# Kernel optimization log

Measured on AMD Instinct MI355X. Metric: run time of the kernel, lower is better.

Reference implementation:

```python
import jax, jax.numpy as jnp
import numpy as np

B, C_IN, C_KEY, C_VAL, C_OUT = 1, 64, 32, 64, 64
H = W = D = 64
SCALE = 8


def setup_inputs() -> dict:
    key = jax.random.key(0)
    ks = jax.random.split(key, 4)
    init = lambda k, shape, fan: jax.random.normal(k, shape, jnp.float32) * (fan ** -0.5)
    return {
        "x": jax.random.normal(ks[0], (B, C_IN, H, W, D), jnp.float32),
        "w_key": init(ks[1], (C_KEY, C_IN), C_IN),
        "b_key": jnp.zeros((C_KEY,), jnp.float32),
        "w_value": init(ks[2], (C_VAL, C_IN), C_IN),
        "b_value": jnp.zeros((C_VAL,), jnp.float32),
        "w_out": init(ks[3], (C_OUT, C_VAL), C_VAL),
        "b_out": jnp.zeros((C_OUT,), jnp.float32),
        "scale": SCALE,
    }


def _proj(t, wgt, bias):
    # 1x1x1 Conv3d == pointwise channel matmul
    return jnp.einsum('bchwd,oc->bohwd', t, wgt) + bias[None, :, None, None, None]


def _windows(t, s):
    # [B,C,H,W,D] -> [B, s^3 windows, hb*wb*db tokens, C]
    b, c, h, w, d = t.shape
    hb, wb, db = h // s, w // s, d // s
    t = t.reshape(b, c, s, hb, s, wb, s, db)
    t = t.transpose(0, 2, 4, 6, 3, 5, 7, 1)
    return t.reshape(b, s * s * s, hb * wb * db, c), (hb, wb, db)


def _unwindows(t, s, blk):
    hb, wb, db = blk
    b, c = t.shape[0], t.shape[-1]
    t = t.reshape(b, s, s, s, hb, wb, db, c)
    t = t.transpose(0, 7, 1, 4, 2, 5, 3, 6)
    return t.reshape(b, c, s * hb, s * wb, s * db)


def reference(x, w_key, b_key, w_value, b_value, w_out, b_out, scale):
    # f_query = f_key (shared module in the original)
    k_full = _proj(x, w_key, b_key)
    v_full = _proj(x, w_value, b_value)
    qw, blk = _windows(k_full, scale)
    kw = qw  # shared projection -> query == key
    vw, _ = _windows(v_full, scale)
    sim = jnp.einsum('bnlc,bnmc->bnlm', qw, kw) * (qw.shape[-1] ** -0.5)
    sim = jax.nn.softmax(sim, axis=-1)
    ctx = jnp.einsum('bnlm,bnmc->bnlc', sim, vw)
    ctx = _unwindows(ctx, scale, blk)
    return _proj(ctx, w_out, b_out)
```

## Files before the change

kernel.cpp:

```cpp
#include <hip/hip_runtime.h>

typedef unsigned short u16;
typedef __bf16 bf16x8 __attribute__((ext_vector_type(8)));
typedef float f32x16 __attribute__((ext_vector_type(16)));

union B8 { bf16x8 v; u16 s[8]; unsigned u[4]; uint4 u4; };

__device__ __forceinline__ unsigned cvtpk(float a, float b) {
    unsigned r;
    asm("v_cvt_pk_bf16_f32 %0, %1, %2" : "=v"(r) : "v"(a), "v"(b));
    return r;
}
__device__ __forceinline__ float ex2(float x) { return __builtin_amdgcn_exp2f(x); }
__device__ __forceinline__ void swap32(unsigned &a, unsigned &b) {
    asm("v_permlane32_swap_b32 %0, %1" : "+v"(a), "+v"(b));
}
__device__ __forceinline__ B8 load_w8(const float* __restrict__ p, float s) {
    float4 lo = ((const float4*)p)[0];
    float4 hi = ((const float4*)p)[1];
    B8 r;
    r.u[0] = cvtpk(lo.x * s, lo.y * s);
    r.u[1] = cvtpk(lo.z * s, lo.w * s);
    r.u[2] = cvtpk(hi.x * s, hi.y * s);
    r.u[3] = cvtpk(hi.z * s, hi.w * s);
    return r;
}
__device__ __forceinline__ f32x16 mfma32(const B8 a, const B8 b, f32x16 c) {
    return __builtin_amdgcn_mfma_f32_32x32x16_bf16(a.v, b.v, c, 0, 0, 0);
}
__device__ __forceinline__ int kidx(int row, int sl) {
    return row * 32 + (((sl ^ (row >> 1)) & 3) << 3);
}
__device__ __forceinline__ void build_b(const float* p, B8& b0, B8& b1) {
    unsigned c0 = cvtpk(p[0], p[1]),   c1 = cvtpk(p[2], p[3]);
    unsigned c2 = cvtpk(p[4], p[5]),   c3 = cvtpk(p[6], p[7]);
    unsigned c4 = cvtpk(p[8], p[9]),   c5 = cvtpk(p[10], p[11]);
    unsigned c6 = cvtpk(p[12], p[13]), c7 = cvtpk(p[14], p[15]);
    swap32(c0, c2); swap32(c1, c3); swap32(c4, c6); swap32(c5, c7);
    b0.u[0] = c0; b0.u[1] = c1; b0.u[2] = c2; b0.u[3] = c3;
    b1.u[0] = c4; b1.u[1] = c5; b1.u[2] = c6; b1.u[3] = c7;
}

#define VOFF 16384
#define XOFF 49664
#define NSM  68096

__global__ __launch_bounds__(1024, 4)
void psab_fused(const float* __restrict__ x,
                const float* __restrict__ wk, const float* __restrict__ bk,
                const float* __restrict__ wv, const float* __restrict__ bv,
                const float* __restrict__ wo, const float* __restrict__ bo,
                float* __restrict__ out)
{
    __shared__ __align__(16) u16 smem[NSM];
    const int t    = threadIdx.x;
    const int lane = t & 63;
    const int wid  = t >> 6;
    const int cl   = lane & 31;
    const int h5   = lane >> 5;

    const int bid = blockIdx.x;
    const int n   = (bid & 7) * 64 + (bid >> 3);
    const int sh = n >> 6, sw = (n >> 3) & 7, sd = n & 7;
    const size_t base_vox = (size_t)(sh * 8) * 4096 + (size_t)(sw * 8) * 64 + (size_t)(sd * 8);

    const float WSC = 0.50506330f;

    const int pair = wid >> 1;
    const int kv   = wid & 1;

    B8 wB[8];
    float bkv[16];
    float vb0 = 0.f, vb1 = 0.f;
    if (kv == 0) {
#pragma unroll
        for (int kc = 0; kc < 4; ++kc)
            wB[kc] = load_w8(wk + cl * 64 + kc * 16 + h5 * 8, WSC);
#pragma unroll
        for (int r = 0; r < 16; ++r)
            bkv[r] = bk[(r & 3) + 8 * (r >> 2) + 4 * h5] * WSC;
    } else {
#pragma unroll
        for (int nb = 0; nb < 2; ++nb)
#pragma unroll
            for (int kc = 0; kc < 4; ++kc)
                wB[nb * 4 + kc] = load_w8(wv + (nb * 32 + cl) * 64 + kc * 16 + h5 * 8, 1.0f);
        vb0 = bv[cl]; vb1 = bv[32 + cl];
    }

    const f32x16 z16 = {0,0,0,0,0,0,0,0,0,0,0,0,0,0,0,0};

    const int cS = t & 63;
    const int r3 = t >> 6;
    float4 L4[2], H4[2];
#define LDX(cc)                                                                               \
    _Pragma("unroll")                                                                         \
    for (int i = 0; i < 2; ++i) {                                                             \
        const int rr = r3 + i * 16;                                                           \
        const float* gp = x + (size_t)cS * 262144 + base_vox                                  \
                        + ((cc) * 4 + (rr >> 3)) * 4096 + (rr & 7) * 64;                      \
        L4[i] = ((const float4*)gp)[0];                                                       \
        H4[i] = ((const float4*)gp)[1];                                                       \
    }
#define STX()                                                                                 \
    _Pragma("unroll")                                                                         \
    for (int i = 0; i < 2; ++i) {                                                             \
        const int rr = r3 + i * 16;                                                           \
        unsigned a0 = cvtpk(L4[i].x, L4[i].y), a1 = cvtpk(L4[i].z, L4[i].w);                  \
        unsigned a2 = cvtpk(H4[i].x, H4[i].y), a3 = cvtpk(H4[i].z, H4[i].w);                  \
        u16* xp = &smem[XOFF + (rr * 8) * 72 + cS];                                           \
        xp[0 * 72] = (u16)a0; xp[1 * 72] = (u16)(a0 >> 16);                                   \
        xp[2 * 72] = (u16)a1; xp[3 * 72] = (u16)(a1 >> 16);                                   \
        xp[4 * 72] = (u16)a2; xp[5 * 72] = (u16)(a2 >> 16);                                   \
        xp[6 * 72] = (u16)a3; xp[7 * 72] = (u16)(a3 >> 16);                                   \
    }

    LDX(0)
    STX()
    __syncthreads();
    LDX(1)

#pragma unroll
    for (int cc = 0; cc < 2; ++cc) {
        const int tokb = cc * 256 + pair * 32;
        B8 ax[4];
#pragma unroll
        for (int kc = 0; kc < 4; ++kc)
            ax[kc].u4 = *(const uint4*)&smem[XOFF + (pair * 32 + cl) * 72 + kc * 16 + h5 * 8];
        if (kv == 0) {
            f32x16 kd = mfma32(wB[0], ax[0], z16);
            kd = mfma32(wB[1], ax[1], kd);
            kd = mfma32(wB[2], ax[2], kd);
            kd = mfma32(wB[3], ax[3], kd);
            const int trow = tokb + cl;
#pragma unroll
            for (int g = 0; g < 4; ++g) {
                uint2 pk;
                pk.x = cvtpk(kd[4 * g + 0] + bkv[4 * g + 0], kd[4 * g + 1] + bkv[4 * g + 1]);
                pk.y = cvtpk(kd[4 * g + 2] + bkv[4 * g + 2], kd[4 * g + 3] + bkv[4 * g + 3]);
                *(uint2*)&smem[kidx(trow, g) + 4 * h5] = pk;
            }
        } else {
#pragma unroll
            for (int nb = 0; nb < 2; ++nb) {
                f32x16 vd = mfma32(ax[0], wB[nb * 4 + 0], z16);
                vd = mfma32(ax[1], wB[nb * 4 + 1], vd);
                vd = mfma32(ax[2], wB[nb * 4 + 2], vd);
                vd = mfma32(ax[3], wB[nb * 4 + 3], vd);
                const int cv = nb * 32 + cl;
                const float vb = nb ? vb1 : vb0;
#pragma unroll
                for (int rq = 0; rq < 4; ++rq) {
                    uint2 pk;
                    pk.x = cvtpk(vd[rq * 4 + 0] + vb, vd[rq * 4 + 1] + vb);
                    pk.y = cvtpk(vd[rq * 4 + 2] + vb, vd[rq * 4 + 3] + vb);
                    *(uint2*)&smem[VOFF + cv * 520 + tokb + rq * 8 + 4 * h5] = pk;
                }
            }
        }
        if (cc == 0) {
            __syncthreads();
            STX()
            __syncthreads();
        }
    }
    __syncthreads();

    B8 qB[2];
#pragma unroll
    for (int kc = 0; kc < 2; ++kc)
        qB[kc].u4 = *(const uint4*)&smem[kidx(wid * 32 + cl, 2 * kc + h5)];

    f32x16 ctx0 = z16, ctx1 = z16;
    float lsum = 0.f;

#pragma unroll 2
    for (int ci = 0; ci < 16; ++ci) {
        const int m0 = ci * 32;
        B8 kA0, kA1, va00, va01, va10, va11;
        kA0.u4  = *(const uint4*)&smem[kidx(m0 + cl, h5)];
        kA1.u4  = *(const uint4*)&smem[kidx(m0 + cl, 2 + h5)];
        va00.u4 = *(const uint4*)&smem[VOFF + cl * 520 + m0 + h5 * 8];
        va01.u4 = *(const uint4*)&smem[VOFF + cl * 520 + m0 + 16 + h5 * 8];
        va10.u4 = *(const uint4*)&smem[VOFF + (32 + cl) * 520 + m0 + h5 * 8];
        va11.u4 = *(const uint4*)&smem[VOFF + (32 + cl) * 520 + m0 + 16 + h5 * 8];

        __builtin_amdgcn_s_setprio(1);
        f32x16 s = mfma32(kA0, qB[0], z16);
        s = mfma32(kA1, qB[1], s);
        __builtin_amdgcn_s_setprio(0);

        float p[16];
#pragma unroll
        for (int i = 0; i < 16; ++i) p[i] = ex2(s[i]);
        lsum += (((p[0]+p[1])+(p[2]+p[3]))+((p[4]+p[5])+(p[6]+p[7])))
              + (((p[8]+p[9])+(p[10]+p[11]))+((p[12]+p[13])+(p[14]+p[15])));
        B8 pb0, pb1;
        build_b(p, pb0, pb1);

        __builtin_amdgcn_s_setprio(1);
        ctx0 = mfma32(va00, pb0, ctx0);
        ctx0 = mfma32(va01, pb1, ctx0);
        ctx1 = mfma32(va10, pb0, ctx1);
        ctx1 = mfma32(va11, pb1, ctx1);
        __builtin_amdgcn_s_setprio(0);
    }

    lsum += __shfl_xor(lsum, 32);
    const float inv = 1.0f / lsum;

    B8 aw[2][4];
#pragma unroll
    for (int cob = 0; cob < 2; ++cob)
#pragma unroll
        for (int kc = 0; kc < 4; ++kc)
            aw[cob][kc] = load_w8(wo + (cob * 32 + cl) * 64 + kc * 16 + h5 * 8, 1.0f);

    float pn[16];
    B8 cq[4];
#pragma unroll
    for (int i = 0; i < 16; ++i) pn[i] = ctx0[i] * inv;
    build_b(pn, cq[0], cq[1]);
#pragma unroll
    for (int i = 0; i < 16; ++i) pn[i] = ctx1[i] * inv;
    build_b(pn, cq[2], cq[3]);

    __syncthreads();

    float* fout = (float*)((char*)smem + wid * 8192);
#pragma unroll
    for (int cob = 0; cob < 2; ++cob) {
        f32x16 od = mfma32(aw[cob][0], cq[0], z16);
        od = mfma32(aw[cob][1], cq[1], od);
        od = mfma32(aw[cob][2], cq[2], od);
        od = mfma32(aw[cob][3], cq[3], od);
#pragma unroll
        for (int r = 0; r < 16; ++r) {
            const int row = cob * 32 + (r & 3) + 8 * (r >> 2) + 4 * h5;
            fout[row * 32 + cl] = od[r];
        }
    }

    float* outw = out + base_vox + (size_t)(wid >> 1) * 4096 + (wid & 1) * 256;
#pragma unroll
    for (int it = 0; it < 8; ++it) {
        const int co = it * 8 + (lane >> 3);
        const int q4 = (lane & 7) * 4;
        float4 v4 = *(const float4*)&fout[co * 32 + q4];
        const float bco = bo[co];
        v4.x += bco; v4.y += bco; v4.z += bco; v4.w += bco;
        const int wb = (lane & 7) >> 1, db0 = (lane & 1) * 4;
        *(float4*)&outw[(size_t)co * 262144 + wb * 64 + db0] = v4;
    }
}

extern "C" void kernel_launch(void* const* d_in, const int* in_sizes, int n_in,
                              void* d_out, int out_size, void* d_ws, size_t ws_size,
                              hipStream_t stream) {
    const float* x  = (const float*)d_in[0];
    const float* wk = (const float*)d_in[1];
    const float* bk = (const float*)d_in[2];
    const float* wv = (const float*)d_in[3];
    const float* bv = (const float*)d_in[4];
    const float* wo = (const float*)d_in[5];
    const float* bo = (const float*)d_in[6];
    float* o = (float*)d_out;
    psab_fused<<<dim3(512), dim3(1024), 0, stream>>>(x, wk, bk, wv, bv, wo, bo, o);
}
```

Measured before the change: 74.32 us.

## Shrink blocks to four waves, each handling four query tiles with shared K/V loads

Cuts each block from 16 to 4 waves. Each wave now computes both the K and V projections for 64 tokens, and in attention it processes four 32-query tiles. This lets each K/V LDS fragment load feed four score and context MFMA groups, reducing LDS traffic per MFMA and the number of barrier participants. The X staging buffer switches from a padded stride-72 layout to an XOR-swizzled stride-64 layout, and the output writeback is restructured to match. In exchange it raises register pressure heavily (eight context accumulators, more weights held in registers) and lowers the number of waves per CU available to hide latency, with launch bounds set to 256 threads.

New measurement: 76.10 us. 1.02x slower.

```diff
diff --git a/kernel.cpp b/kernel.cpp
--- a/kernel.cpp
+++ b/kernel.cpp
@@ -43,9 +43,9 @@
 
 #define VOFF 16384
 #define XOFF 49664
-#define NSM  68096
-
-__global__ __launch_bounds__(1024, 4)
+#define NSM  66048
+
+__global__ __launch_bounds__(256, 1)
 void psab_fused(const float* __restrict__ x,
                 const float* __restrict__ wk, const float* __restrict__ bk,
                 const float* __restrict__ wv, const float* __restrict__ bv,
@@ -66,37 +66,29 @@
 
     const float WSC = 0.50506330f;
 
-    const int pair = wid >> 1;
-    const int kv   = wid & 1;
-
-    B8 wB[8];
+    B8 wkB[4], wvB[2][4];
+#pragma unroll
+    for (int kc = 0; kc < 4; ++kc)
+        wkB[kc] = load_w8(wk + cl * 64 + kc * 16 + h5 * 8, WSC);
+#pragma unroll
+    for (int nb = 0; nb < 2; ++nb)
+#pragma unroll
+        for (int kc = 0; kc < 4; ++kc)
+            wvB[nb][kc] = load_w8(wv + (nb * 32 + cl) * 64 + kc * 16 + h5 * 8, 1.0f);
     float bkv[16];
-    float vb0 = 0.f, vb1 = 0.f;
-    if (kv == 0) {
-#pragma unroll
-        for (int kc = 0; kc < 4; ++kc)
-            wB[kc] = load_w8(wk + cl * 64 + kc * 16 + h5 * 8, WSC);
-#pragma unroll
-        for (int r = 0; r < 16; ++r)
-            bkv[r] = bk[(r & 3) + 8 * (r >> 2) + 4 * h5] * WSC;
-    } else {
-#pragma unroll
-        for (int nb = 0; nb < 2; ++nb)
-#pragma unroll
-            for (int kc = 0; kc < 4; ++kc)
-                wB[nb * 4 + kc] = load_w8(wv + (nb * 32 + cl) * 64 + kc * 16 + h5 * 8, 1.0f);
-        vb0 = bv[cl]; vb1 = bv[32 + cl];
-    }
+#pragma unroll
+    for (int r = 0; r < 16; ++r)
+        bkv[r] = bk[(r & 3) + 8 * (r >> 2) + 4 * h5] * WSC;
+    const float vb0 = bv[cl], vb1 = bv[32 + cl];
 
     const f32x16 z16 = {0,0,0,0,0,0,0,0,0,0,0,0,0,0,0,0};
 
     const int cS = t & 63;
-    const int r3 = t >> 6;
-    float4 L4[2], H4[2];
+    float4 L4[8], H4[8];
 #define LDX(cc)                                                                               \
     _Pragma("unroll")                                                                         \
-    for (int i = 0; i < 2; ++i) {                                                             \
-        const int rr = r3 + i * 16;                                                           \
+    for (int i = 0; i < 8; ++i) {                                                             \
+        const int rr = wid + i * 4;                                                           \
         const float* gp = x + (size_t)cS * 262144 + base_vox                                  \
                         + ((cc) * 4 + (rr >> 3)) * 4096 + (rr & 7) * 64;                      \
         L4[i] = ((const float4*)gp)[0];                                                       \
@@ -104,15 +96,15 @@
     }
 #define STX()                                                                                 \
     _Pragma("unroll")                                                                         \
-    for (int i = 0; i < 2; ++i) {                                                             \
-        const int rr = r3 + i * 16;                                                           \
+    for (int i = 0; i < 8; ++i) {                                                             \
+        const int rr = wid + i * 4;                                                           \
         unsigned a0 = cvtpk(L4[i].x, L4[i].y), a1 = cvtpk(L4[i].z, L4[i].w);                  \
         unsigned a2 = cvtpk(H4[i].x, H4[i].y), a3 = cvtpk(H4[i].z, H4[i].w);                  \
-        u16* xp = &smem[XOFF + (rr * 8) * 72 + cS];                                           \
-        xp[0 * 72] = (u16)a0; xp[1 * 72] = (u16)(a0 >> 16);                                   \
-        xp[2 * 72] = (u16)a1; xp[3 * 72] = (u16)(a1 >> 16);                                   \
-        xp[4 * 72] = (u16)a2; xp[5 * 72] = (u16)(a2 >> 16);                                   \
-        xp[6 * 72] = (u16)a3; xp[7 * 72] = (u16)(a3 >> 16);                                   \
+        const u16 vals[8] = { (u16)a0, (u16)(a0 >> 16), (u16)a1, (u16)(a1 >> 16),             \
+                              (u16)a2, (u16)(a2 >> 16), (u16)a3, (u16)(a3 >> 16) };           \
+        _Pragma("unroll")                                                                     \
+        for (int j = 0; j < 8; ++j)                                                           \
+            smem[XOFF + (rr * 8 + j) * 64 + (((cS >> 3) ^ j) << 3) + (cS & 7)] = vals[j];     \
     }
 
     LDX(0)
@@ -122,16 +114,20 @@
 
 #pragma unroll
     for (int cc = 0; cc < 2; ++cc) {
-        const int tokb = cc * 256 + pair * 32;
-        B8 ax[4];
-#pragma unroll
-        for (int kc = 0; kc < 4; ++kc)
-            ax[kc].u4 = *(const uint4*)&smem[XOFF + (pair * 32 + cl) * 72 + kc * 16 + h5 * 8];
-        if (kv == 0) {
-            f32x16 kd = mfma32(wB[0], ax[0], z16);
-            kd = mfma32(wB[1], ax[1], kd);
-            kd = mfma32(wB[2], ax[2], kd);
-            kd = mfma32(wB[3], ax[3], kd);
+#pragma unroll
+        for (int sb = 0; sb < 2; ++sb) {
+            const int ltok = wid * 64 + sb * 32 + cl;
+            const int tokb = cc * 256 + wid * 64 + sb * 32;
+            B8 ax[4];
+#pragma unroll
+            for (int kc = 0; kc < 4; ++kc) {
+                const int slot = (kc * 2 + h5) ^ (ltok & 7);
+                ax[kc].u4 = *(const uint4*)&smem[XOFF + ltok * 64 + (slot << 3)];
+            }
+            f32x16 kd = mfma32(wkB[0], ax[0], z16);
+            kd = mfma32(wkB[1], ax[1], kd);
+            kd = mfma32(wkB[2], ax[2], kd);
+            kd = mfma32(wkB[3], ax[3], kd);
             const int trow = tokb + cl;
 #pragma unroll
             for (int g = 0; g < 4; ++g) {
@@ -140,13 +136,12 @@
                 pk.y = cvtpk(kd[4 * g + 2] + bkv[4 * g + 2], kd[4 * g + 3] + bkv[4 * g + 3]);
                 *(uint2*)&smem[kidx(trow, g) + 4 * h5] = pk;
             }
-        } else {
 #pragma unroll
             for (int nb = 0; nb < 2; ++nb) {
-                f32x16 vd = mfma32(ax[0], wB[nb * 4 + 0], z16);
-                vd = mfma32(ax[1], wB[nb * 4 + 1], vd);
-                vd = mfma32(ax[2], wB[nb * 4 + 2], vd);
-                vd = mfma32(ax[3], wB[nb * 4 + 3], vd);
+                f32x16 vd = mfma32(ax[0], wvB[nb][0], z16);
+                vd = mfma32(ax[1], wvB[nb][1], vd);
+                vd = mfma32(ax[2], wvB[nb][2], vd);
+                vd = mfma32(ax[3], wvB[nb][3], vd);
                 const int cv = nb * 32 + cl;
                 const float vb = nb ? vb1 : vb0;
 #pragma unroll
@@ -166,13 +161,31 @@
     }
     __syncthreads();
 
-    B8 qB[2];
-#pragma unroll
-    for (int kc = 0; kc < 2; ++kc)
-        qB[kc].u4 = *(const uint4*)&smem[kidx(wid * 32 + cl, 2 * kc + h5)];
-
-    f32x16 ctx0 = z16, ctx1 = z16;
-    float lsum = 0.f;
+    B8 qB[4][2];
+#pragma unroll
+    for (int qb = 0; qb < 4; ++qb)
+#pragma unroll
+        for (int kc = 0; kc < 2; ++kc)
+            qB[qb][kc].u4 = *(const uint4*)&smem[kidx(wid * 128 + qb * 32 + cl, 2 * kc + h5)];
+
+    f32x16 ctx00 = z16, ctx01 = z16, ctx10 = z16, ctx11 = z16;
+    f32x16 ctx20 = z16, ctx21 = z16, ctx30 = z16, ctx31 = z16;
+    float ls0 = 0.f, ls1 = 0.f, ls2 = 0.f, ls3 = 0.f;
+
+#define SM(qb, sv, c0, c1)                                                                    \
+    {                                                                                         \
+        float p[16];                                                                          \
+        _Pragma("unroll")                                                                     \
+        for (int i = 0; i < 16; ++i) p[i] = ex2(sv[i]);                                       \
+        ls##qb += (((p[0]+p[1])+(p[2]+p[3]))+((p[4]+p[5])+(p[6]+p[7])))                       \
+                + (((p[8]+p[9])+(p[10]+p[11]))+((p[12]+p[13])+(p[14]+p[15])));                \
+        B8 pb0, pb1;                                                                          \
+        build_b(p, pb0, pb1);                                                                 \
+        c0 = mfma32(va00, pb0, c0);                                                           \
+        c0 = mfma32(va01, pb1, c0);                                                           \
+        c1 = mfma32(va10, pb0, c1);                                                           \
+        c1 = mfma32(va11, pb1, c1);                                                           \
+    }
 
 #pragma unroll 2
     for (int ci = 0; ci < 16; ++ci) {
@@ -185,29 +198,23 @@
         va10.u4 = *(const uint4*)&smem[VOFF + (32 + cl) * 520 + m0 + h5 * 8];
         va11.u4 = *(const uint4*)&smem[VOFF + (32 + cl) * 520 + m0 + 16 + h5 * 8];
 
-        __builtin_amdgcn_s_setprio(1);
-        f32x16 s = mfma32(kA0, qB[0], z16);
-        s = mfma32(kA1, qB[1], s);
-        __builtin_amdgcn_s_setprio(0);
-
-        float p[16];
-#pragma unroll
-        for (int i = 0; i < 16; ++i) p[i] = ex2(s[i]);
-        lsum += (((p[0]+p[1])+(p[2]+p[3]))+((p[4]+p[5])+(p[6]+p[7])))
-              + (((p[8]+p[9])+(p[10]+p[11]))+((p[12]+p[13])+(p[14]+p[15])));
-        B8 pb0, pb1;
-        build_b(p, pb0, pb1);
-
-        __builtin_amdgcn_s_setprio(1);
-        ctx0 = mfma32(va00, pb0, ctx0);
-        ctx0 = mfma32(va01, pb1, ctx0);
-        ctx1 = mfma32(va10, pb0, ctx1);
-        ctx1 = mfma32(va11, pb1, ctx1);
-        __builtin_amdgcn_s_setprio(0);
-    }
-
-    lsum += __shfl_xor(lsum, 32);
-    const float inv = 1.0f / lsum;
+        f32x16 s0 = mfma32(kA0, qB[0][0], z16); s0 = mfma32(kA1, qB[0][1], s0);
+        f32x16 s1 = mfma32(kA0, qB[1][0], z16); s1 = mfma32(kA1, qB[1][1], s1);
+        f32x16 s2 = mfma32(kA0, qB[2][0], z16); s2 = mfma32(kA1, qB[2][1], s2);
+        f32x16 s3 = mfma32(kA0, qB[3][0], z16); s3 = mfma32(kA1, qB[3][1], s3);
+
+        SM(0, s0, ctx00, ctx01)
+        SM(1, s1, ctx10, ctx11)
+        SM(2, s2, ctx20, ctx21)
+        SM(3, s3, ctx30, ctx31)
+    }
+
+    ls0 += __shfl_xor(ls0, 32);
+    ls1 += __shfl_xor(ls1, 32);
+    ls2 += __shfl_xor(ls2, 32);
+    ls3 += __shfl_xor(ls3, 32);
+    const float inv0 = 1.0f / ls0, inv1 = 1.0f / ls1;
+    const float inv2 = 1.0f / ls2, inv3 = 1.0f / ls3;
 
     B8 aw[2][4];
 #pragma unroll
@@ -217,40 +224,66 @@
             aw[cob][kc] = load_w8(wo + (cob * 32 + cl) * 64 + kc * 16 + h5 * 8, 1.0f);
 
     float pn[16];
-    B8 cq[4];
-#pragma unroll
-    for (int i = 0; i < 16; ++i) pn[i] = ctx0[i] * inv;
-    build_b(pn, cq[0], cq[1]);
-#pragma unroll
-    for (int i = 0; i < 16; ++i) pn[i] = ctx1[i] * inv;
-    build_b(pn, cq[2], cq[3]);
+    B8 cq0[4], cq1[4], cq2[4], cq3[4];
+#pragma unroll
+    for (int i = 0; i < 16; ++i) pn[i] = ctx00[i] * inv0;
+    build_b(pn, cq0[0], cq0[1]);
+#pragma unroll
+    for (int i = 0; i < 16; ++i) pn[i] = ctx01[i] * inv0;
+    build_b(pn, cq0[2], cq0[3]);
+#pragma unroll
+    for (int i = 0; i < 16; ++i) pn[i] = ctx10[i] * inv1;
+    build_b(pn, cq1[0], cq1[1]);
+#pragma unroll
+    for (int i = 0; i < 16; ++i) pn[i] = ctx11[i] * inv1;
+    build_b(pn, cq1[2], cq1[3]);
+#pragma unroll
+    for (int i = 0; i < 16; ++i) pn[i] = ctx20[i] * inv2;
+    build_b(pn, cq2[0], cq2[1]);
+#pragma unroll
+    for (int i = 0; i < 16; ++i) pn[i] = ctx21[i] * inv2;
+    build_b(pn, cq2[2], cq2[3]);
+#pragma unroll
+    for (int i = 0; i < 16; ++i) pn[i] = ctx30[i] * inv3;
+    build_b(pn, cq3[0], cq3[1]);
+#pragma unroll
+    for (int i = 0; i < 16; ++i) pn[i] = ctx31[i] * inv3;
+    build_b(pn, cq3[2], cq3[3]);
 
     __syncthreads();
 
-    float* fout = (float*)((char*)smem + wid * 8192);
-#pragma unroll
-    for (int cob = 0; cob < 2; ++cob) {
-        f32x16 od = mfma32(aw[cob][0], cq[0], z16);
-        od = mfma32(aw[cob][1], cq[1], od);
-        od = mfma32(aw[cob][2], cq[2], od);
-        od = mfma32(aw[cob][3], cq[3], od);
-#pragma unroll
-        for (int r = 0; r < 16; ++r) {
-            const int row = cob * 32 + (r & 3) + 8 * (r >> 2) + 4 * h5;
-            fout[row * 32 + cl] = od[r];
-        }
-    }
-
-    float* outw = out + base_vox + (size_t)(wid >> 1) * 4096 + (wid & 1) * 256;
-#pragma unroll
-    for (int it = 0; it < 8; ++it) {
-        const int co = it * 8 + (lane >> 3);
-        const int q4 = (lane & 7) * 4;
-        float4 v4 = *(const float4*)&fout[co * 32 + q4];
+    float* fout = (float*)((char*)smem + wid * 32768);
+#define OPROJ(qb, cq)                                                                         \
+    _Pragma("unroll")                                                                         \
+    for (int cob = 0; cob < 2; ++cob) {                                                       \
+        f32x16 od = mfma32(aw[cob][0], cq[0], z16);                                           \
+        od = mfma32(aw[cob][1], cq[1], od);                                                   \
+        od = mfma32(aw[cob][2], cq[2], od);                                                   \
+        od = mfma32(aw[cob][3], cq[3], od);                                                   \
+        _Pragma("unroll")                                                                     \
+        for (int r = 0; r < 16; ++r) {                                                        \
+            const int row = cob * 32 + (r & 3) + 8 * (r >> 2) + 4 * h5;                       \
+            fout[row * 128 + (qb) * 32 + cl] = od[r];                                         \
+        }                                                                                     \
+    }
+    OPROJ(0, cq0)
+    OPROJ(1, cq1)
+    OPROJ(2, cq2)
+    OPROJ(3, cq3)
+
+    float* outw = out + base_vox + (size_t)(wid * 2) * 4096;
+    const int qg  = lane & 31;
+    const int co0 = lane >> 5;
+    const int hbl = qg >> 4;
+    const int wb  = (qg >> 1) & 7;
+    const int db0 = (qg & 1) * 4;
+#pragma unroll
+    for (int it = 0; it < 32; ++it) {
+        const int co = it * 2 + co0;
+        float4 v4 = *(const float4*)&fout[co * 128 + qg * 4];
         const float bco = bo[co];
         v4.x += bco; v4.y += bco; v4.z += bco; v4.w += bco;
-        const int wb = (lane & 7) >> 1, db0 = (lane & 1) * 4;
-        *(float4*)&outw[(size_t)co * 262144 + wb * 64 + db0] = v4;
+        *(float4*)&outw[(size_t)co * 262144 + hbl * 4096 + wb * 64 + db0] = v4;
     }
 }
 
@@ -265,5 +298,5 @@
     const float* wo = (const float*)d_in[5];
     const float* bo = (const float*)d_in[6];
     float* o = (float*)d_out;
-    psab_fused<<<dim3(512), dim3(1024), 0, stream>>>(x, wk, bk, wv, bv, wo, bo, o);
-}
+    psab_fused<<<dim3(512), dim3(256), 0, stream>>>(x, wk, bk, wv, bv, wo, bo, o);
+}
```

## Split each window across two 512-thread blocks with half-resident V projection

Applied to the files above, without the earlier changes.

Each window's 512 queries are now split over two 512-thread blocks. Every block recomputes the full K projection and computes V in two halves: the second half is projected between two attention passes so the V buffer holds only 256 tokens. The x staging tile in LDS is removed; x is gathered straight from global memory into MFMA operand registers. A swizzle is added to the V layout and the output staging buffer is padded, to cut LDS bank conflicts. The smaller LDS footprint and block size are meant to raise occupancy, at the cost of duplicated K/V projection work, duplicated x reads, and strided scalar global gathers.

Result: slower. 196.0 us (+163.7%).

```diff
diff --git a/kernel.cpp b/kernel.cpp
--- a/kernel.cpp
+++ b/kernel.cpp
@@ -31,6 +31,7 @@
 __device__ __forceinline__ int kidx(int row, int sl) {
     return row * 32 + (((sl ^ (row >> 1)) & 3) << 3);
 }
+#define SWZV(cv) (((cv) ^ ((cv) >> 3)) & 3)
 __device__ __forceinline__ void build_b(const float* p, B8& b0, B8& b1) {
     unsigned c0 = cvtpk(p[0], p[1]),   c1 = cvtpk(p[2], p[3]);
     unsigned c2 = cvtpk(p[4], p[5]),   c3 = cvtpk(p[6], p[7]);
@@ -42,10 +43,9 @@
 }
 
 #define VOFF 16384
-#define XOFF 49664
-#define NSM  68096
-
-__global__ __launch_bounds__(1024, 4)
+#define NSM  36864
+
+__global__ __launch_bounds__(512, 4)
 void psab_fused(const float* __restrict__ x,
                 const float* __restrict__ wk, const float* __restrict__ bk,
                 const float* __restrict__ wv, const float* __restrict__ bv,
@@ -60,108 +60,93 @@
     const int h5   = lane >> 5;
 
     const int bid = blockIdx.x;
-    const int n   = (bid & 7) * 64 + (bid >> 3);
+    const int xcd = bid & 7;
+    const int ii  = bid >> 3;
+    const int n   = xcd * 64 + (ii >> 1);
+    const int qh  = ii & 1;
     const int sh = n >> 6, sw = (n >> 3) & 7, sd = n & 7;
     const size_t base_vox = (size_t)(sh * 8) * 4096 + (size_t)(sw * 8) * 64 + (size_t)(sd * 8);
+    const float* xb = x + base_vox;
 
     const float WSC = 0.50506330f;
-
-    const int pair = wid >> 1;
-    const int kv   = wid & 1;
-
-    B8 wB[8];
-    float bkv[16];
-    float vb0 = 0.f, vb1 = 0.f;
-    if (kv == 0) {
+    const f32x16 z16 = {0,0,0,0,0,0,0,0,0,0,0,0,0,0,0,0};
+
+    B8 ax[4];
+#define GATHER(G)                                                                             \
+    {                                                                                         \
+        const int vox = ((G) >> 1) * 4096 + (((G) & 1) * 4 + (cl >> 3)) * 64 + (cl & 7);      \
+        const float* px = xb + vox;                                                           \
+        _Pragma("unroll")                                                                     \
+        for (int kc = 0; kc < 4; ++kc) {                                                      \
+            float f0 = px[(size_t)(kc * 16 + h5 * 8 + 0) * 262144];                           \
+            float f1 = px[(size_t)(kc * 16 + h5 * 8 + 1) * 262144];                           \
+            float f2 = px[(size_t)(kc * 16 + h5 * 8 + 2) * 262144];                           \
+            float f3 = px[(size_t)(kc * 16 + h5 * 8 + 3) * 262144];                           \
+            float f4 = px[(size_t)(kc * 16 + h5 * 8 + 4) * 262144];                           \
+            float f5 = px[(size_t)(kc * 16 + h5 * 8 + 5) * 262144];                           \
+            float f6 = px[(size_t)(kc * 16 + h5 * 8 + 6) * 262144];                           \
+            float f7 = px[(size_t)(kc * 16 + h5 * 8 + 7) * 262144];                           \
+            ax[kc].u[0] = cvtpk(f0, f1); ax[kc].u[1] = cvtpk(f2, f3);                         \
+            ax[kc].u[2] = cvtpk(f4, f5); ax[kc].u[3] = cvtpk(f6, f7);                         \
+        }                                                                                     \
+    }
+
+#define VPROJ(TOKL)                                                                           \
+    _Pragma("unroll")                                                                         \
+    for (int nb = 0; nb < 2; ++nb) {                                                          \
+        f32x16 vd = mfma32(ax[0], wvB[nb][0], z16);                                           \
+        vd = mfma32(ax[1], wvB[nb][1], vd);                                                   \
+        vd = mfma32(ax[2], wvB[nb][2], vd);                                                   \
+        vd = mfma32(ax[3], wvB[nb][3], vd);                                                   \
+        const int cv = nb * 32 + cl;                                                          \
+        const float vb = nb ? vb1 : vb0;                                                      \
+        const int swv = SWZV(cv);                                                             \
+        _Pragma("unroll")                                                                     \
+        for (int rq = 0; rq < 4; ++rq) {                                                      \
+            uint2 pk;                                                                         \
+            pk.x = cvtpk(vd[rq * 4 + 0] + vb, vd[rq * 4 + 1] + vb);                           \
+            pk.y = cvtpk(vd[rq * 4 + 2] + vb, vd[rq * 4 + 3] + vb);                           \
+            const int off = (TOKL) + rq * 8 + 4 * h5;                                         \
+            *(uint2*)&smem[VOFF + cv * 264 + (((off >> 3) ^ swv) << 3) + (off & 7)] = pk;     \
+        }                                                                                     \
+    }
+
+    {
+        B8 wkA[4];
 #pragma unroll
         for (int kc = 0; kc < 4; ++kc)
-            wB[kc] = load_w8(wk + cl * 64 + kc * 16 + h5 * 8, WSC);
+            wkA[kc] = load_w8(wk + cl * 64 + kc * 16 + h5 * 8, WSC);
+        float bkv[16];
 #pragma unroll
         for (int r = 0; r < 16; ++r)
             bkv[r] = bk[(r & 3) + 8 * (r >> 2) + 4 * h5] * WSC;
-    } else {
-#pragma unroll
-        for (int nb = 0; nb < 2; ++nb)
-#pragma unroll
-            for (int kc = 0; kc < 4; ++kc)
-                wB[nb * 4 + kc] = load_w8(wv + (nb * 32 + cl) * 64 + kc * 16 + h5 * 8, 1.0f);
-        vb0 = bv[cl]; vb1 = bv[32 + cl];
-    }
-
-    const f32x16 z16 = {0,0,0,0,0,0,0,0,0,0,0,0,0,0,0,0};
-
-    const int cS = t & 63;
-    const int r3 = t >> 6;
-    float4 L4[2], H4[2];
-#define LDX(cc)                                                                               \
-    _Pragma("unroll")                                                                         \
-    for (int i = 0; i < 2; ++i) {                                                             \
-        const int rr = r3 + i * 16;                                                           \
-        const float* gp = x + (size_t)cS * 262144 + base_vox                                  \
-                        + ((cc) * 4 + (rr >> 3)) * 4096 + (rr & 7) * 64;                      \
-        L4[i] = ((const float4*)gp)[0];                                                       \
-        H4[i] = ((const float4*)gp)[1];                                                       \
-    }
-#define STX()                                                                                 \
-    _Pragma("unroll")                                                                         \
-    for (int i = 0; i < 2; ++i) {                                                             \
-        const int rr = r3 + i * 16;                                                           \
-        unsigned a0 = cvtpk(L4[i].x, L4[i].y), a1 = cvtpk(L4[i].z, L4[i].w);                  \
-        unsigned a2 = cvtpk(H4[i].x, H4[i].y), a3 = cvtpk(H4[i].z, H4[i].w);                  \
-        u16* xp = &smem[XOFF + (rr * 8) * 72 + cS];                                           \
-        xp[0 * 72] = (u16)a0; xp[1 * 72] = (u16)(a0 >> 16);                                   \
-        xp[2 * 72] = (u16)a1; xp[3 * 72] = (u16)(a1 >> 16);                                   \
-        xp[4 * 72] = (u16)a2; xp[5 * 72] = (u16)(a2 >> 16);                                   \
-        xp[6 * 72] = (u16)a3; xp[7 * 72] = (u16)(a3 >> 16);                                   \
-    }
-
-    LDX(0)
-    STX()
-    __syncthreads();
-    LDX(1)
-
-#pragma unroll
-    for (int cc = 0; cc < 2; ++cc) {
-        const int tokb = cc * 256 + pair * 32;
-        B8 ax[4];
-#pragma unroll
-        for (int kc = 0; kc < 4; ++kc)
-            ax[kc].u4 = *(const uint4*)&smem[XOFF + (pair * 32 + cl) * 72 + kc * 16 + h5 * 8];
-        if (kv == 0) {
-            f32x16 kd = mfma32(wB[0], ax[0], z16);
-            kd = mfma32(wB[1], ax[1], kd);
-            kd = mfma32(wB[2], ax[2], kd);
-            kd = mfma32(wB[3], ax[3], kd);
-            const int trow = tokb + cl;
-#pragma unroll
-            for (int g = 0; g < 4; ++g) {
+        B8 wvB[2][4];
+        float vb0 = 0.f, vb1 = 0.f;
+        if (wid < 4) {
+#pragma unroll
+            for (int nb = 0; nb < 2; ++nb)
+#pragma unroll
+                for (int kc = 0; kc < 4; ++kc)
+                    wvB[nb][kc] = load_w8(wv + (nb * 32 + cl) * 64 + kc * 16 + h5 * 8, 1.0f);
+            vb0 = bv[cl]; vb1 = bv[32 + cl];
+        }
+#pragma unroll
+        for (int sb = 0; sb < 2; ++sb) {
+            const int g = wid * 2 + sb;
+            GATHER(g)
+            f32x16 kd = mfma32(wkA[0], ax[0], z16);
+            kd = mfma32(wkA[1], ax[1], kd);
+            kd = mfma32(wkA[2], ax[2], kd);
+            kd = mfma32(wkA[3], ax[3], kd);
+            const int trow = g * 32 + cl;
+#pragma unroll
+            for (int g2 = 0; g2 < 4; ++g2) {
                 uint2 pk;
-                pk.x = cvtpk(kd[4 * g + 0] + bkv[4 * g + 0], kd[4 * g + 1] + bkv[4 * g + 1]);
-                pk.y = cvtpk(kd[4 * g + 2] + bkv[4 * g + 2], kd[4 * g + 3] + bkv[4 * g + 3]);
-                *(uint2*)&smem[kidx(trow, g) + 4 * h5] = pk;
+                pk.x = cvtpk(kd[4 * g2 + 0] + bkv[4 * g2 + 0], kd[4 * g2 + 1] + bkv[4 * g2 + 1]);
+                pk.y = cvtpk(kd[4 * g2 + 2] + bkv[4 * g2 + 2], kd[4 * g2 + 3] + bkv[4 * g2 + 3]);
+                *(uint2*)&smem[kidx(trow, g2) + 4 * h5] = pk;
             }
-        } else {
-#pragma unroll
-            for (int nb = 0; nb < 2; ++nb) {
-                f32x16 vd = mfma32(ax[0], wB[nb * 4 + 0], z16);
-                vd = mfma32(ax[1], wB[nb * 4 + 1], vd);
-                vd = mfma32(ax[2], wB[nb * 4 + 2], vd);
-                vd = mfma32(ax[3], wB[nb * 4 + 3], vd);
-                const int cv = nb * 32 + cl;
-                const float vb = nb ? vb1 : vb0;
-#pragma unroll
-                for (int rq = 0; rq < 4; ++rq) {
-                    uint2 pk;
-                    pk.x = cvtpk(vd[rq * 4 + 0] + vb, vd[rq * 4 + 1] + vb);
-                    pk.y = cvtpk(vd[rq * 4 + 2] + vb, vd[rq * 4 + 3] + vb);
-                    *(uint2*)&smem[VOFF + cv * 520 + tokb + rq * 8 + 4 * h5] = pk;
-                }
-            }
-        }
-        if (cc == 0) {
-            __syncthreads();
-            STX()
-            __syncthreads();
+            if (wid < 4) { VPROJ(g * 32) }
         }
     }
     __syncthreads();
@@ -169,42 +154,59 @@
     B8 qB[2];
 #pragma unroll
     for (int kc = 0; kc < 2; ++kc)
-        qB[kc].u4 = *(const uint4*)&smem[kidx(wid * 32 + cl, 2 * kc + h5)];
+        qB[kc].u4 = *(const uint4*)&smem[kidx(qh * 256 + wid * 32 + cl, 2 * kc + h5)];
 
     f32x16 ctx0 = z16, ctx1 = z16;
     float lsum = 0.f;
 
-#pragma unroll 2
-    for (int ci = 0; ci < 16; ++ci) {
-        const int m0 = ci * 32;
-        B8 kA0, kA1, va00, va01, va10, va11;
-        kA0.u4  = *(const uint4*)&smem[kidx(m0 + cl, h5)];
-        kA1.u4  = *(const uint4*)&smem[kidx(m0 + cl, 2 + h5)];
-        va00.u4 = *(const uint4*)&smem[VOFF + cl * 520 + m0 + h5 * 8];
-        va01.u4 = *(const uint4*)&smem[VOFF + cl * 520 + m0 + 16 + h5 * 8];
-        va10.u4 = *(const uint4*)&smem[VOFF + (32 + cl) * 520 + m0 + h5 * 8];
-        va11.u4 = *(const uint4*)&smem[VOFF + (32 + cl) * 520 + m0 + 16 + h5 * 8];
-
-        __builtin_amdgcn_s_setprio(1);
-        f32x16 s = mfma32(kA0, qB[0], z16);
-        s = mfma32(kA1, qB[1], s);
-        __builtin_amdgcn_s_setprio(0);
-
-        float p[16];
-#pragma unroll
-        for (int i = 0; i < 16; ++i) p[i] = ex2(s[i]);
-        lsum += (((p[0]+p[1])+(p[2]+p[3]))+((p[4]+p[5])+(p[6]+p[7])))
-              + (((p[8]+p[9])+(p[10]+p[11]))+((p[12]+p[13])+(p[14]+p[15])));
-        B8 pb0, pb1;
-        build_b(p, pb0, pb1);
-
-        __builtin_amdgcn_s_setprio(1);
-        ctx0 = mfma32(va00, pb0, ctx0);
-        ctx0 = mfma32(va01, pb1, ctx0);
-        ctx1 = mfma32(va10, pb0, ctx1);
-        ctx1 = mfma32(va11, pb1, ctx1);
-        __builtin_amdgcn_s_setprio(0);
-    }
+#define ATTN_PASS(CI0, CI1, MOFF)                                                             \
+    _Pragma("unroll 2")                                                                       \
+    for (int ci = (CI0); ci < (CI1); ++ci) {                                                  \
+        const int m0 = ci * 32;                                                               \
+        const int s0i = ((m0 - (MOFF)) >> 3) + h5;                                            \
+        B8 kA0, kA1, va00, va01, va10, va11;                                                  \
+        kA0.u4  = *(const uint4*)&smem[kidx(m0 + cl, h5)];                                    \
+        kA1.u4  = *(const uint4*)&smem[kidx(m0 + cl, 2 + h5)];                                \
+        va00.u4 = *(const uint4*)&smem[VOFF + cl * 264 + ((s0i ^ SWZV(cl)) << 3)];            \
+        va01.u4 = *(const uint4*)&smem[VOFF + cl * 264 + (((s0i + 2) ^ SWZV(cl)) << 3)];      \
+        va10.u4 = *(const uint4*)&smem[VOFF + (32 + cl) * 264 + ((s0i ^ SWZV(32 + cl)) << 3)];\
+        va11.u4 = *(const uint4*)&smem[VOFF + (32 + cl) * 264 + (((s0i + 2) ^ SWZV(32 + cl)) << 3)]; \
+        f32x16 s = mfma32(kA0, qB[0], z16);                                                   \
+        s = mfma32(kA1, qB[1], s);                                                            \
+        float p[16];                                                                          \
+        _Pragma("unroll")                                                                     \
+        for (int i2 = 0; i2 < 16; ++i2) p[i2] = ex2(s[i2]);                                   \
+        lsum += (((p[0]+p[1])+(p[2]+p[3]))+((p[4]+p[5])+(p[6]+p[7])))                         \
+              + (((p[8]+p[9])+(p[10]+p[11]))+((p[12]+p[13])+(p[14]+p[15])));                  \
+        B8 pb0, pb1;                                                                          \
+        build_b(p, pb0, pb1);                                                                 \
+        ctx0 = mfma32(va00, pb0, ctx0);                                                       \
+        ctx0 = mfma32(va01, pb1, ctx0);                                                       \
+        ctx1 = mfma32(va10, pb0, ctx1);                                                       \
+        ctx1 = mfma32(va11, pb1, ctx1);                                                       \
+    }
+
+    ATTN_PASS(0, 8, 0)
+    __syncthreads();
+
+    if (wid >= 4) {
+        B8 wvB[2][4];
+#pragma unroll
+        for (int nb = 0; nb < 2; ++nb)
+#pragma unroll
+            for (int kc = 0; kc < 4; ++kc)
+                wvB[nb][kc] = load_w8(wv + (nb * 32 + cl) * 64 + kc * 16 + h5 * 8, 1.0f);
+        const float vb0 = bv[cl], vb1 = bv[32 + cl];
+#pragma unroll
+        for (int sb = 0; sb < 2; ++sb) {
+            const int g = wid * 2 + sb;
+            GATHER(g)
+            VPROJ(g * 32 - 256)
+        }
+    }
+    __syncthreads();
+
+    ATTN_PASS(8, 16, 256)
 
     lsum += __shfl_xor(lsum, 32);
     const float inv = 1.0f / lsum;
@@ -215,7 +217,6 @@
 #pragma unroll
         for (int kc = 0; kc < 4; ++kc)
             aw[cob][kc] = load_w8(wo + (cob * 32 + cl) * 64 + kc * 16 + h5 * 8, 1.0f);
-
     float pn[16];
     B8 cq[4];
 #pragma unroll
@@ -227,7 +228,7 @@
 
     __syncthreads();
 
-    float* fout = (float*)((char*)smem + wid * 8192);
+    float* fout = (float*)((char*)smem + wid * 9216);
 #pragma unroll
     for (int cob = 0; cob < 2; ++cob) {
         f32x16 od = mfma32(aw[cob][0], cq[0], z16);
@@ -237,19 +238,21 @@
 #pragma unroll
         for (int r = 0; r < 16; ++r) {
             const int row = cob * 32 + (r & 3) + 8 * (r >> 2) + 4 * h5;
-            fout[row * 32 + cl] = od[r];
-        }
-    }
-
-    float* outw = out + base_vox + (size_t)(wid >> 1) * 4096 + (wid & 1) * 256;
+            fout[row * 36 + cl] = od[r];
+        }
+    }
+
+    const int hb = qh * 4 + (wid >> 1);
+    const int sb = wid & 1;
+    float* outw = out + base_vox + (size_t)hb * 4096 + sb * 4 * 64;
+    const int q4 = (lane & 7) * 4;
+    const int wb = q4 >> 3, db0 = q4 & 7;
 #pragma unroll
     for (int it = 0; it < 8; ++it) {
         const int co = it * 8 + (lane >> 3);
-        const int q4 = (lane & 7) * 4;
-        float4 v4 = *(const float4*)&fout[co * 32 + q4];
+        float4 v4 = *(const float4*)&fout[co * 36 + q4];
         const float bco = bo[co];
         v4.x += bco; v4.y += bco; v4.z += bco; v4.w += bco;
-        const int wb = (lane & 7) >> 1, db0 = (lane & 1) * 4;
         *(float4*)&outw[(size_t)co * 262144 + wb * 64 + db0] = v4;
     }
 }
@@ -265,5 +268,5 @@
     const float* wo = (const float*)d_in[5];
     const float* bo = (const float*)d_in[6];
     float* o = (float*)d_out;
-    psab_fused<<<dim3(512), dim3(1024), 0, stream>>>(x, wk, bk, wv, bv, wo, bo, o);
-}
+    psab_fused<<<dim3(1024), dim3(512), 0, stream>>>(x, wk, bk, wv, bv, wo, bo, o);
+}
```
